# Kernel tuning notes

Measured on AMD Instinct MI355X. Metric: run time of the kernel, lower is better.

The kernel has to match this reference:

```python
import jax, jax.numpy as jnp
import numpy as np

N = 200000   # real nodes
P = 10       # num_parts (virtual nodes)
IN = 256     # in_channels
HID = 256    # hidden_channels
DCD = 256    # decode_channels (use_jk=False -> == hidden)
OUT = 64     # out_channels


def layer_norm(x, g, b, eps=1e-5):
    mu = jnp.mean(x, axis=-1, keepdims=True)
    var = jnp.var(x, axis=-1, keepdims=True)
    return (x - mu) * jax.lax.rsqrt(var + eps) * g + b


def setup_inputs() -> dict:
    key = jax.random.key(0)
    ks = jax.random.split(key, 16)
    s = lambda d: 1.0 / np.sqrt(d)
    return {
        "x": jax.random.normal(ks[0], (N + P, IN), dtype=jnp.float32),
        "mapping": jax.random.randint(ks[1], (N,), 0, P, dtype=jnp.int32),
        "vnode_embed": jax.random.normal(ks[2], (P, IN), dtype=jnp.float32),
        "vnode_bias_hid": 0.1 * jax.random.normal(ks[3], (P, HID), dtype=jnp.float32),
        "vnode_bias_dcd": 0.1 * jax.random.normal(ks[4], (P, DCD), dtype=jnp.float32),
        "W_in2hid": s(IN) * jax.random.normal(ks[5], (IN, HID), dtype=jnp.float32),
        "b_in2hid": jnp.zeros((HID,), dtype=jnp.float32),
        "g_ln_hid": jnp.ones((HID,), dtype=jnp.float32),
        "b_ln_hid": jnp.zeros((HID,), dtype=jnp.float32),
        "W_enc": s(HID) * jax.random.normal(ks[6], (HID, DCD), dtype=jnp.float32),
        "b_enc": jnp.zeros((DCD,), dtype=jnp.float32),
        "g_ln_enc": jnp.ones((DCD,), dtype=jnp.float32),
        "b_ln_enc": jnp.zeros((DCD,), dtype=jnp.float32),
        "W_aggr": s(2 * DCD) * jax.random.normal(ks[7], (2 * DCD, DCD), dtype=jnp.float32),
        "b_aggr": jnp.zeros((DCD,), dtype=jnp.float32),
        "W_out": s(DCD) * jax.random.normal(ks[8], (DCD, OUT), dtype=jnp.float32),
        "b_out": jnp.zeros((OUT,), dtype=jnp.float32),
    }


def reference(x, mapping, vnode_embed, vnode_bias_hid, vnode_bias_dcd,
              W_in2hid, b_in2hid, g_ln_hid, b_ln_hid,
              W_enc, b_enc, g_ln_enc, b_ln_enc,
              W_aggr, b_aggr, W_out, b_out):
    p = vnode_embed.shape[0]
    n = x.shape[0] - p
    # overwrite virtual-node rows with learned embeddings
    x = x.at[-p:].set(vnode_embed)
    # in2hid -> LayerNorm -> ELU
    x = jax.nn.elu(layer_norm(x @ W_in2hid + b_in2hid, g_ln_hid, b_ln_hid))
    x = x.at[-p:].add(vnode_bias_hid)
    # encoder stub: single linear hidden->decode with ELU (loss := 0)
    x = jax.nn.elu(x @ W_enc + b_enc)
    # decode-stage virtual-node bias
    x = x.at[-p:].add(vnode_bias_dcd)
    v_x = x[-p:]                      # [P, DCD]
    gathered = v_x[mapping]           # irregular gather of virtual rows, [N, DCD]
    n_x = jnp.concatenate([x[:n], gathered], axis=1)   # [N, 2*DCD]
    n_x = jax.nn.elu(layer_norm(n_x @ W_aggr + b_aggr, g_ln_enc, b_ln_enc))
    # dropout: eval mode -> identity
    full = jnp.concatenate([n_x, v_x], axis=0)
    y = full @ W_out + b_out
    out = y[:n]                       # [N, OUT]
    return out
```

## Files before the change

### kernel.cpp

```cpp
#include <hip/hip_runtime.h>
#include <hip/hip_bf16.h>
#include <math.h>

typedef unsigned short u16;
typedef unsigned int u32;
typedef __attribute__((ext_vector_type(8))) short bf16x8;
typedef __attribute__((ext_vector_type(4))) float f32x4;
typedef __attribute__((ext_vector_type(4))) int i32x4;

#define PV 10

__device__ __forceinline__ float bf2f(u16 u){
  union{unsigned int i; float f;} v; v.i = ((unsigned int)u)<<16; return v.f;
}
__device__ __forceinline__ u16 f2bf(float f){
  union{float f; unsigned int i;} v; v.f = f;
  unsigned int r = (v.i + 0x7FFFu + ((v.i>>16)&1u))>>16;
  return (u16)r;
}
__device__ __forceinline__ u32 cvtpk(float lo, float hi){
  u32 r; asm("v_cvt_pk_bf16_f32 %0, %1, %2" : "=v"(r) : "v"(lo), "v"(hi)); return r;
}
__device__ __forceinline__ float eluf(float z){
  return z > 0.f ? z : (__expf(z) - 1.f);
}
__device__ __forceinline__ float ldp(const void* p, int i, int f32f){
  return f32f ? ((const float*)p)[i] : bf2f(((const u16*)p)[i]);
}
__device__ __forceinline__ int swz(int row, int cb){
  int m = ((row & 7) << 4) ^ ((row & 8) << 2);
  return (row << 9) + (cb ^ m);
}

__global__ void k_sniff(const u16* __restrict__ x, int* __restrict__ flag){
  int t = threadIdx.x;
  u16 u = x[2*t];
  int e = (u >> 7) & 0xFF;
  int sane = (e >= 113 && e <= 134) ? 1 : 0;
  unsigned long long b = __ballot(sane);
  if (t == 0) *flag = (__popcll(b) < 32) ? 1 : 0;
}

__global__ void k_fragpack(const int* __restrict__ flagp,
                           const void* __restrict__ W1, const void* __restrict__ W2,
                           const void* __restrict__ Wa, const void* __restrict__ Wo,
                           u16* __restrict__ W1F, u16* __restrict__ W2F,
                           u16* __restrict__ WaF, u16* __restrict__ WoF)
{
  const int f = *flagp;
  int idx = blockIdx.x * 256 + threadIdx.x;
  if (idx < 196608) {
    int local = idx & 65535;
    int which = idx >> 16;
    int j = local & 7;
    int fid = local >> 3;
    int lane = fid & 63, q = lane & 15, g = lane >> 4;
    int n = (fid >> 6) & 3;
    int s = (fid >> 8) & 7;
    int w = (fid >> 11) & 3;
    int col = 64*w + 16*n + q;
    int k = 32*s + 8*g + j;
    const void* src = which == 0 ? W1 : (which == 1 ? W2 : Wa);
    u16* dst = which == 0 ? W1F : (which == 1 ? W2F : WaF);
    dst[local] = f2bf(ldp(src, k*256 + col, f));
  } else if (idx < 212992) {
    int local = idx - 196608;
    int j = local & 7;
    int fid = local >> 3;
    int lane = fid & 63, q = lane & 15, g = lane >> 4;
    int n = (fid >> 6) & 3;
    int s = (fid >> 8) & 7;
    int col = 16*n + q;
    int k = 32*s + 8*g + j;
    WoF[local] = f2bf(ldp(Wo, k*64 + col, f));
  }
}

__global__ void k_vnode(const int* __restrict__ flagp,
                        const void* __restrict__ embed, const void* __restrict__ W1,
                        const void* __restrict__ b1, const void* __restrict__ g1, const void* __restrict__ bb1,
                        const void* __restrict__ vbh,
                        const void* __restrict__ W2, const void* __restrict__ b2,
                        const void* __restrict__ vbd,
                        const void* __restrict__ Wa, const void* __restrict__ ba,
                        float* __restrict__ vg)
{
  __shared__ float buf[PV][256];
  __shared__ float st[PV][2];
  const int f = *flagp;
  const int t = threadIdx.x;
  const int lane = t & 63;
  const int w = t >> 6;

  for (int r=0;r<PV;r++) buf[r][t] = ldp(embed, r*256 + t, f);
  __syncthreads();

  float acc[PV];

  #pragma unroll
  for (int r=0;r<PV;r++) acc[r] = 0.f;
  for (int k8=0;k8<32;k8++){
    float wf[8];
    #pragma unroll
    for (int j=0;j<8;j++) wf[j] = ldp(W1, (k8*8+j)*256 + t, f);
    #pragma unroll
    for (int r=0;r<PV;r++){
      f32x4 a0 = *(const f32x4*)(&buf[r][k8*8]);
      f32x4 a1 = *(const f32x4*)(&buf[r][k8*8+4]);
      acc[r] = fmaf(a0[0],wf[0],acc[r]); acc[r] = fmaf(a0[1],wf[1],acc[r]);
      acc[r] = fmaf(a0[2],wf[2],acc[r]); acc[r] = fmaf(a0[3],wf[3],acc[r]);
      acc[r] = fmaf(a1[0],wf[4],acc[r]); acc[r] = fmaf(a1[1],wf[5],acc[r]);
      acc[r] = fmaf(a1[2],wf[6],acc[r]); acc[r] = fmaf(a1[3],wf[7],acc[r]);
    }
  }
  {
    float bv = ldp(b1, t, f);
    #pragma unroll
    for (int r=0;r<PV;r++) acc[r] += bv;
  }
  __syncthreads();
  #pragma unroll
  for (int r=0;r<PV;r++) buf[r][t] = acc[r];
  __syncthreads();
  for (int r = w; r < PV; r += 4){
    float v0=buf[r][lane], v1=buf[r][lane+64], v2=buf[r][lane+128], v3=buf[r][lane+192];
    float s = v0+v1+v2+v3;
    float ss = v0*v0+v1*v1+v2*v2+v3*v3;
    #pragma unroll
    for (int off=1; off<64; off<<=1){ s += __shfl_xor(s,off,64); ss += __shfl_xor(ss,off,64); }
    if (lane==0){
      float mu = s*(1.f/256.f);
      float var = ss*(1.f/256.f) - mu*mu;
      st[r][0]=mu; st[r][1]=rsqrtf(var+1e-5f);
    }
  }
  __syncthreads();
  {
    float gv = ldp(g1,t,f), bbv = ldp(bb1,t,f);
    #pragma unroll
    for (int r=0;r<PV;r++){
      float v = (acc[r]-st[r][0])*st[r][1]*gv + bbv;
      buf[r][t] = eluf(v) + ldp(vbh, r*256+t, f);
    }
  }
  __syncthreads();

  #pragma unroll
  for (int r=0;r<PV;r++) acc[r] = 0.f;
  for (int k8=0;k8<32;k8++){
    float wf[8];
    #pragma unroll
    for (int j=0;j<8;j++) wf[j] = ldp(W2, (k8*8+j)*256 + t, f);
    #pragma unroll
    for (int r=0;r<PV;r++){
      f32x4 a0 = *(const f32x4*)(&buf[r][k8*8]);
      f32x4 a1 = *(const f32x4*)(&buf[r][k8*8+4]);
      acc[r] = fmaf(a0[0],wf[0],acc[r]); acc[r] = fmaf(a0[1],wf[1],acc[r]);
      acc[r] = fmaf(a0[2],wf[2],acc[r]); acc[r] = fmaf(a0[3],wf[3],acc[r]);
      acc[r] = fmaf(a1[0],wf[4],acc[r]); acc[r] = fmaf(a1[1],wf[5],acc[r]);
      acc[r] = fmaf(a1[2],wf[6],acc[r]); acc[r] = fmaf(a1[3],wf[7],acc[r]);
    }
  }
  __syncthreads();
  {
    float bv = ldp(b2,t,f);
    #pragma unroll
    for (int r=0;r<PV;r++) buf[r][t] = eluf(acc[r]+bv) + ldp(vbd, r*256+t, f);
  }
  __syncthreads();

  #pragma unroll
  for (int r=0;r<PV;r++) acc[r] = 0.f;
  for (int k8=0;k8<32;k8++){
    float wf[8];
    #pragma unroll
    for (int j=0;j<8;j++) wf[j] = ldp(Wa, (256 + k8*8+j)*256 + t, f);
    #pragma unroll
    for (int r=0;r<PV;r++){
      f32x4 a0 = *(const f32x4*)(&buf[r][k8*8]);
      f32x4 a1 = *(const f32x4*)(&buf[r][k8*8+4]);
      acc[r] = fmaf(a0[0],wf[0],acc[r]); acc[r] = fmaf(a0[1],wf[1],acc[r]);
      acc[r] = fmaf(a0[2],wf[2],acc[r]); acc[r] = fmaf(a0[3],wf[3],acc[r]);
      acc[r] = fmaf(a1[0],wf[4],acc[r]); acc[r] = fmaf(a1[1],wf[5],acc[r]);
      acc[r] = fmaf(a1[2],wf[6],acc[r]); acc[r] = fmaf(a1[3],wf[7],acc[r]);
    }
  }
  {
    float bv = ldp(ba,t,f);
    #pragma unroll
    for (int r=0;r<PV;r++) vg[r*256+t] = acc[r] + bv;
  }
}

__device__ __forceinline__ void ln_rows(f32x4 (&acc)[4][4], float2 (*part)[4], float2* stats,
                                        int tid, int wid, int q, int g)
{
  #pragma unroll
  for (int m=0;m<4;m++){
    #pragma unroll
    for (int j=0;j<4;j++){
      float s1=0.f, s2=0.f;
      #pragma unroll
      for (int n=0;n<4;n++){ float v = acc[m][n][j]; s1+=v; s2+=v*v; }
      s1 += __shfl_xor(s1,1,64); s2 += __shfl_xor(s2,1,64);
      s1 += __shfl_xor(s1,2,64); s2 += __shfl_xor(s2,2,64);
      s1 += __shfl_xor(s1,4,64); s2 += __shfl_xor(s2,4,64);
      s1 += __shfl_xor(s1,8,64); s2 += __shfl_xor(s2,8,64);
      if (q == 0) part[16*m + 4*g + j][wid] = make_float2(s1, s2);
    }
  }
  __syncthreads();
  if (tid < 64){
    float s=0.f, ss=0.f;
    #pragma unroll
    for (int w=0;w<4;w++){ float2 p = part[tid][w]; s+=p.x; ss+=p.y; }
    float mu = s*(1.f/256.f);
    float var = ss*(1.f/256.f) - mu*mu;
    stats[tid] = make_float2(mu, rsqrtf(var + 1e-5f));
  }
  __syncthreads();
}

__global__ __launch_bounds__(256, 3) void k_main(
    const int* __restrict__ flagp,
    const void* __restrict__ x, const int* __restrict__ mapping,
    const void* __restrict__ b1, const void* __restrict__ g1, const void* __restrict__ bb1,
    const void* __restrict__ b2,
    const void* __restrict__ g3, const void* __restrict__ bb3,
    const void* __restrict__ bo,
    const u16* __restrict__ W1F, const u16* __restrict__ W2F,
    const u16* __restrict__ WaF, const u16* __restrict__ WoF,
    const float* __restrict__ vg, void* __restrict__ out)
{
  __shared__ __align__(16) u16 Abuf[64*256];
  __shared__ float2 part[64][4];
  __shared__ float2 stats[64];
  __shared__ int maplds[64];

  const int f = *flagp;
  const int tid = threadIdx.x;
  const int wid = tid >> 6;
  const int lane = tid & 63;
  const int q = lane & 15;
  const int g = lane >> 4;
  const int R0 = blockIdx.x * 64;

  if (f) {
    const float* xr = (const float*)x + (size_t)R0 * 256;
    #pragma unroll
    for (int i=0;i<8;i++){
      int c = tid + 256*i;
      int row = c >> 5;
      int cb  = (c & 31) << 4;
      int e0  = (c & 31) << 3;
      float4 a = *(const float4*)(xr + row*256 + e0);
      float4 b = *(const float4*)(xr + row*256 + e0 + 4);
      union { u32 u[4]; i32x4 v; } pk;
      pk.u[0]=cvtpk(a.x,a.y); pk.u[1]=cvtpk(a.z,a.w);
      pk.u[2]=cvtpk(b.x,b.y); pk.u[3]=cvtpk(b.z,b.w);
      *(i32x4*)((char*)Abuf + swz(row, cb)) = pk.v;
    }
  } else {
    const u16* xr = (const u16*)x + (size_t)R0 * 256;
    #pragma unroll
    for (int i=0;i<8;i++){
      int c = tid + 256*i;
      int row = c >> 5;
      int cb  = (c & 31) << 4;
      i32x4 v = *(const i32x4*)(xr + row*256 + ((c&31)<<3));
      *(i32x4*)((char*)Abuf + swz(row, cb)) = v;
    }
  }
  if (tid < 64){
    int mv = mapping[R0 + tid];
    maplds[tid] = mv < 0 ? 0 : (mv > PV-1 ? PV-1 : mv);
  }
  __syncthreads();

  f32x4 acc[4][4];
  const int fbase = wid*16384 + lane*8;

  {
    #pragma unroll
    for (int n=0;n<4;n++){
      float bv = ldp(b1, 64*wid + 16*n + q, f);
      #pragma unroll
      for (int m=0;m<4;m++) acc[m][n] = (f32x4){bv,bv,bv,bv};
    }
    #pragma unroll
    for (int s=0;s<8;s++){
      bf16x8 af[4], bw[4];
      #pragma unroll
      for (int m=0;m<4;m++) af[m] = *(const bf16x8*)((const char*)Abuf + swz(16*m+q, 64*s+16*g));
      #pragma unroll
      for (int n=0;n<4;n++) bw[n] = *(const bf16x8*)(W1F + fbase + (s*4+n)*512);
      #pragma unroll
      for (int m=0;m<4;m++){
        #pragma unroll
        for (int n=0;n<4;n++)
          acc[m][n] = __builtin_amdgcn_mfma_f32_16x16x32_bf16(af[m], bw[n], acc[m][n], 0,0,0);
      }
    }
  }
  ln_rows(acc, part, stats, tid, wid, q, g);
  {
    float gam[4], bet[4];
    #pragma unroll
    for (int n=0;n<4;n++){ int col = 64*wid+16*n+q; gam[n]=ldp(g1,col,f); bet[n]=ldp(bb1,col,f); }
    #pragma unroll
    for (int m=0;m<4;m++){
      #pragma unroll
      for (int n=0;n<4;n++){
        float v[4];
        #pragma unroll
        for (int j=0;j<4;j++){
          float2 st = stats[16*m + 4*g + j];
          v[j] = eluf((acc[m][n][j] - st.x) * st.y * gam[n] + bet[n]);
        }
        u32 u01 = cvtpk(v[0],v[1]), u23 = cvtpk(v[2],v[3]);
        int col2 = (64*wid+16*n+q)<<1;
        *(u16*)((char*)Abuf + swz(16*m+4*g+0, col2)) = (u16)u01;
        *(u16*)((char*)Abuf + swz(16*m+4*g+1, col2)) = (u16)(u01>>16);
        *(u16*)((char*)Abuf + swz(16*m+4*g+2, col2)) = (u16)u23;
        *(u16*)((char*)Abuf + swz(16*m+4*g+3, col2)) = (u16)(u23>>16);
      }
    }
  }
  __syncthreads();

  {
    #pragma unroll
    for (int n=0;n<4;n++){
      float bv = ldp(b2, 64*wid + 16*n + q, f);
      #pragma unroll
      for (int m=0;m<4;m++) acc[m][n] = (f32x4){bv,bv,bv,bv};
    }
    #pragma unroll
    for (int s=0;s<8;s++){
      bf16x8 af[4], bw[4];
      #pragma unroll
      for (int m=0;m<4;m++) af[m] = *(const bf16x8*)((const char*)Abuf + swz(16*m+q, 64*s+16*g));
      #pragma unroll
      for (int n=0;n<4;n++) bw[n] = *(const bf16x8*)(W2F + fbase + (s*4+n)*512);
      #pragma unroll
      for (int m=0;m<4;m++){
        #pragma unroll
        for (int n=0;n<4;n++)
          acc[m][n] = __builtin_amdgcn_mfma_f32_16x16x32_bf16(af[m], bw[n], acc[m][n], 0,0,0);
      }
    }
  }
  __syncthreads();
  {
    #pragma unroll
    for (int m=0;m<4;m++){
      #pragma unroll
      for (int n=0;n<4;n++){
        float v[4];
        #pragma unroll
        for (int j=0;j<4;j++) v[j] = eluf(acc[m][n][j]);
        u32 u01 = cvtpk(v[0],v[1]), u23 = cvtpk(v[2],v[3]);
        int col2 = (64*wid+16*n+q)<<1;
        *(u16*)((char*)Abuf + swz(16*m+4*g+0, col2)) = (u16)u01;
        *(u16*)((char*)Abuf + swz(16*m+4*g+1, col2)) = (u16)(u01>>16);
        *(u16*)((char*)Abuf + swz(16*m+4*g+2, col2)) = (u16)u23;
        *(u16*)((char*)Abuf + swz(16*m+4*g+3, col2)) = (u16)(u23>>16);
      }
    }
  }
  __syncthreads();

  {
    #pragma unroll
    for (int m=0;m<4;m++){
      int mp[4];
      #pragma unroll
      for (int j=0;j<4;j++) mp[j] = maplds[16*m + 4*g + j];
      #pragma unroll
      for (int n=0;n<4;n++){
        int col = 64*wid + 16*n + q;
        #pragma unroll
        for (int j=0;j<4;j++) acc[m][n][j] = vg[mp[j]*256 + col];
      }
    }
    #pragma unroll
    for (int s=0;s<8;s++){
      bf16x8 af[4], bw[4];
      #pragma unroll
      for (int m=0;m<4;m++) af[m] = *(const bf16x8*)((const char*)Abuf + swz(16*m+q, 64*s+16*g));
      #pragma unroll
      for (int n=0;n<4;n++) bw[n] = *(const bf16x8*)(WaF + fbase + (s*4+n)*512);
      #pragma unroll
      for (int m=0;m<4;m++){
        #pragma unroll
        for (int n=0;n<4;n++)
          acc[m][n] = __builtin_amdgcn_mfma_f32_16x16x32_bf16(af[m], bw[n], acc[m][n], 0,0,0);
      }
    }
  }
  ln_rows(acc, part, stats, tid, wid, q, g);
  {
    float gam[4], bet[4];
    #pragma unroll
    for (int n=0;n<4;n++){ int col = 64*wid+16*n+q; gam[n]=ldp(g3,col,f); bet[n]=ldp(bb3,col,f); }
    #pragma unroll
    for (int m=0;m<4;m++){
      #pragma unroll
      for (int n=0;n<4;n++){
        float v[4];
        #pragma unroll
        for (int j=0;j<4;j++){
          float2 st = stats[16*m + 4*g + j];
          v[j] = eluf((acc[m][n][j] - st.x) * st.y * gam[n] + bet[n]);
        }
        u32 u01 = cvtpk(v[0],v[1]), u23 = cvtpk(v[2],v[3]);
        int col2 = (64*wid+16*n+q)<<1;
        *(u16*)((char*)Abuf + swz(16*m+4*g+0, col2)) = (u16)u01;
        *(u16*)((char*)Abuf + swz(16*m+4*g+1, col2)) = (u16)(u01>>16);
        *(u16*)((char*)Abuf + swz(16*m+4*g+2, col2)) = (u16)u23;
        *(u16*)((char*)Abuf + swz(16*m+4*g+3, col2)) = (u16)(u23>>16);
      }
    }
  }
  __syncthreads();

  {
    f32x4 a4[4];
    #pragma unroll
    for (int n=0;n<4;n++){ float bv = ldp(bo, 16*n+q, f); a4[n] = (f32x4){bv,bv,bv,bv}; }
    #pragma unroll
    for (int s=0;s<8;s++){
      bf16x8 af = *(const bf16x8*)((const char*)Abuf + swz(16*wid+q, 64*s+16*g));
      #pragma unroll
      for (int n=0;n<4;n++){
        bf16x8 bw = *(const bf16x8*)(WoF + (s*4+n)*512 + lane*8);
        a4[n] = __builtin_amdgcn_mfma_f32_16x16x32_bf16(af, bw, a4[n], 0,0,0);
      }
    }
    if (f){
      __syncthreads();
      float* obuf = (float*)Abuf;
      #pragma unroll
      for (int n=0;n<4;n++){
        #pragma unroll
        for (int j=0;j<4;j++)
          obuf[(16*wid + 4*g + j)*68 + 16*n + q] = a4[n][j];
      }
      __syncthreads();
      int row = tid >> 2, c0 = (tid & 3) * 16;
      const float* src = obuf + row*68 + c0;
      float* dst = (float*)out + (size_t)(R0 + row)*64 + c0;
      f32x4 v0 = *(const f32x4*)(src);
      f32x4 v1 = *(const f32x4*)(src + 4);
      f32x4 v2 = *(const f32x4*)(src + 8);
      f32x4 v3 = *(const f32x4*)(src + 12);
      __builtin_nontemporal_store(v0, (f32x4*)(dst));
      __builtin_nontemporal_store(v1, (f32x4*)(dst + 4));
      __builtin_nontemporal_store(v2, (f32x4*)(dst + 8));
      __builtin_nontemporal_store(v3, (f32x4*)(dst + 12));
    } else {
      u16* outh = (u16*)out;
      #pragma unroll
      for (int n=0;n<4;n++){
        #pragma unroll
        for (int j=0;j<4;j++){
          int grow = R0 + 16*wid + 4*g + j;
          outh[(size_t)grow*64 + 16*n + q] = f2bf(a4[n][j]);
        }
      }
    }
  }
}

extern "C" void kernel_launch(void* const* d_in, const int* in_sizes, int n_in,
                              void* d_out, int out_size, void* d_ws, size_t ws_size,
                              hipStream_t stream)
{
  const void* x    = d_in[0];
  const int* mapping = (const int*)d_in[1];
  const void* embed= d_in[2];
  const void* vbh  = d_in[3];
  const void* vbd  = d_in[4];
  const void* W1   = d_in[5];
  const void* b1   = d_in[6];
  const void* g1   = d_in[7];
  const void* bb1  = d_in[8];
  const void* W2   = d_in[9];
  const void* b2   = d_in[10];
  const void* g3   = d_in[11];
  const void* bb3  = d_in[12];
  const void* Wa   = d_in[13];
  const void* ba   = d_in[14];
  const void* Wo   = d_in[15];
  const void* bo   = d_in[16];

  char* ws = (char*)d_ws;
  int* flagp = (int*)ws;
  u16* W1F = (u16*)(ws + 4096);
  u16* W2F = (u16*)(ws + 4096 + 131072);
  u16* WaF = (u16*)(ws + 4096 + 262144);
  u16* WoF = (u16*)(ws + 4096 + 393216);
  float* vg = (float*)(ws + 4096 + 425984);

  const int N = in_sizes[1];

  k_sniff<<<1, 64, 0, stream>>>((const u16*)x, flagp);
  k_fragpack<<<832, 256, 0, stream>>>(flagp, W1, W2, Wa, Wo, W1F, W2F, WaF, WoF);
  k_vnode<<<1, 256, 0, stream>>>(flagp, embed, W1, b1, g1, bb1, vbh, W2, b2, vbd, Wa, ba, vg);
  k_main<<<N/64, 256, 0, stream>>>(flagp, x, mapping, b1, g1, bb1, b2, g3, bb3, bo,
                                   W1F, W2F, WaF, WoF, vg, (void*)d_out);
}
```

Measured before the change: 352.5 us.

## Give each wave its own 16 rows and all 256 columns to drop block barriers

The main kernel is restructured so that each wave owns 16 rows and computes all 256 output columns itself, with a private 8KB LDS slice. Previously four waves split the columns of a 64-row tile. LayerNorm statistics are now reduced entirely with in-wave shuffles, which removes the cross-wave partial-sum buffer and every __syncthreads. The weight fragment packing is relaid out to match the new full-width per-wave access. In exchange, every wave must stream the full weight matrices from global/L2 instead of a quarter of them, and each A fragment is reused over 16 column tiles instead of 4.

New measurement: 413.2 us. 1.17x slower.

```diff
diff --git a/kernel.cpp b/kernel.cpp
--- a/kernel.cpp
+++ b/kernel.cpp
@@ -55,10 +55,9 @@
     int j = local & 7;
     int fid = local >> 3;
     int lane = fid & 63, q = lane & 15, g = lane >> 4;
-    int n = (fid >> 6) & 3;
-    int s = (fid >> 8) & 7;
-    int w = (fid >> 11) & 3;
-    int col = 64*w + 16*n + q;
+    int n = (fid >> 6) & 15;
+    int s = (fid >> 10) & 7;
+    int col = 16*n + q;
     int k = 32*s + 8*g + j;
     const void* src = which == 0 ? W1 : (which == 1 ? W2 : Wa);
     u16* dst = which == 0 ? W1F : (which == 1 ? W2F : WaF);
@@ -192,35 +191,6 @@
   }
 }
 
-__device__ __forceinline__ void ln_rows(f32x4 (&acc)[4][4], float2 (*part)[4], float2* stats,
-                                        int tid, int wid, int q, int g)
-{
-  #pragma unroll
-  for (int m=0;m<4;m++){
-    #pragma unroll
-    for (int j=0;j<4;j++){
-      float s1=0.f, s2=0.f;
-      #pragma unroll
-      for (int n=0;n<4;n++){ float v = acc[m][n][j]; s1+=v; s2+=v*v; }
-      s1 += __shfl_xor(s1,1,64); s2 += __shfl_xor(s2,1,64);
-      s1 += __shfl_xor(s1,2,64); s2 += __shfl_xor(s2,2,64);
-      s1 += __shfl_xor(s1,4,64); s2 += __shfl_xor(s2,4,64);
-      s1 += __shfl_xor(s1,8,64); s2 += __shfl_xor(s2,8,64);
-      if (q == 0) part[16*m + 4*g + j][wid] = make_float2(s1, s2);
-    }
-  }
-  __syncthreads();
-  if (tid < 64){
-    float s=0.f, ss=0.f;
-    #pragma unroll
-    for (int w=0;w<4;w++){ float2 p = part[tid][w]; s+=p.x; ss+=p.y; }
-    float mu = s*(1.f/256.f);
-    float var = ss*(1.f/256.f) - mu*mu;
-    stats[tid] = make_float2(mu, rsqrtf(var + 1e-5f));
-  }
-  __syncthreads();
-}
-
 __global__ __launch_bounds__(256, 3) void k_main(
     const int* __restrict__ flagp,
     const void* __restrict__ x, const int* __restrict__ mapping,
@@ -232,10 +202,7 @@
     const u16* __restrict__ WaF, const u16* __restrict__ WoF,
     const float* __restrict__ vg, void* __restrict__ out)
 {
-  __shared__ __align__(16) u16 Abuf[64*256];
-  __shared__ float2 part[64][4];
-  __shared__ float2 stats[64];
-  __shared__ int maplds[64];
+  __shared__ __align__(16) u16 Sall[4*4096];
 
   const int f = *flagp;
   const int tid = threadIdx.x;
@@ -243,186 +210,168 @@
   const int lane = tid & 63;
   const int q = lane & 15;
   const int g = lane >> 4;
-  const int R0 = blockIdx.x * 64;
-
-  if (f) {
-    const float* xr = (const float*)x + (size_t)R0 * 256;
-    #pragma unroll
-    for (int i=0;i<8;i++){
-      int c = tid + 256*i;
-      int row = c >> 5;
-      int cb  = (c & 31) << 4;
-      int e0  = (c & 31) << 3;
-      float4 a = *(const float4*)(xr + row*256 + e0);
-      float4 b = *(const float4*)(xr + row*256 + e0 + 4);
-      union { u32 u[4]; i32x4 v; } pk;
-      pk.u[0]=cvtpk(a.x,a.y); pk.u[1]=cvtpk(a.z,a.w);
-      pk.u[2]=cvtpk(b.x,b.y); pk.u[3]=cvtpk(b.z,b.w);
-      *(i32x4*)((char*)Abuf + swz(row, cb)) = pk.v;
-    }
-  } else {
-    const u16* xr = (const u16*)x + (size_t)R0 * 256;
-    #pragma unroll
-    for (int i=0;i<8;i++){
-      int c = tid + 256*i;
-      int row = c >> 5;
-      int cb  = (c & 31) << 4;
-      i32x4 v = *(const i32x4*)(xr + row*256 + ((c&31)<<3));
-      *(i32x4*)((char*)Abuf + swz(row, cb)) = v;
-    }
-  }
-  if (tid < 64){
-    int mv = mapping[R0 + tid];
-    maplds[tid] = mv < 0 ? 0 : (mv > PV-1 ? PV-1 : mv);
-  }
-  __syncthreads();
-
-  f32x4 acc[4][4];
-  const int fbase = wid*16384 + lane*8;
-
-  {
-    #pragma unroll
-    for (int n=0;n<4;n++){
-      float bv = ldp(b1, 64*wid + 16*n + q, f);
-      #pragma unroll
-      for (int m=0;m<4;m++) acc[m][n] = (f32x4){bv,bv,bv,bv};
-    }
+  const int R0 = blockIdx.x * 64 + wid * 16;
+  u16* S = Sall + wid * 4096;
+
+  {
+    int sr = lane >> 2;
+    int sc = (lane & 3) * 64;
+    if (f){
+      const float* xr = (const float*)x + (size_t)(R0 + sr)*256 + sc;
+      #pragma unroll
+      for (int i=0;i<8;i++){
+        float4 a = *(const float4*)(xr + i*8);
+        float4 b = *(const float4*)(xr + i*8 + 4);
+        union{ u32 u[4]; i32x4 v; } pk;
+        pk.u[0]=cvtpk(a.x,a.y); pk.u[1]=cvtpk(a.z,a.w);
+        pk.u[2]=cvtpk(b.x,b.y); pk.u[3]=cvtpk(b.z,b.w);
+        *(i32x4*)((char*)S + swz(sr, (sc + i*8)*2)) = pk.v;
+      }
+    } else {
+      const u16* xr = (const u16*)x + (size_t)(R0 + sr)*256 + sc;
+      #pragma unroll
+      for (int i=0;i<8;i++){
+        i32x4 v = *(const i32x4*)(xr + i*8);
+        *(i32x4*)((char*)S + swz(sr, (sc + i*8)*2)) = v;
+      }
+    }
+  }
+
+  f32x4 acc[16];
+
+  {
+    #pragma unroll
+    for (int n=0;n<16;n++){ float bv = ldp(b1, 16*n+q, f); acc[n] = (f32x4){bv,bv,bv,bv}; }
     #pragma unroll
     for (int s=0;s<8;s++){
-      bf16x8 af[4], bw[4];
-      #pragma unroll
-      for (int m=0;m<4;m++) af[m] = *(const bf16x8*)((const char*)Abuf + swz(16*m+q, 64*s+16*g));
-      #pragma unroll
-      for (int n=0;n<4;n++) bw[n] = *(const bf16x8*)(W1F + fbase + (s*4+n)*512);
-      #pragma unroll
-      for (int m=0;m<4;m++){
-        #pragma unroll
-        for (int n=0;n<4;n++)
-          acc[m][n] = __builtin_amdgcn_mfma_f32_16x16x32_bf16(af[m], bw[n], acc[m][n], 0,0,0);
-      }
-    }
-  }
-  ln_rows(acc, part, stats, tid, wid, q, g);
-  {
-    float gam[4], bet[4];
-    #pragma unroll
-    for (int n=0;n<4;n++){ int col = 64*wid+16*n+q; gam[n]=ldp(g1,col,f); bet[n]=ldp(bb1,col,f); }
-    #pragma unroll
-    for (int m=0;m<4;m++){
-      #pragma unroll
-      for (int n=0;n<4;n++){
-        float v[4];
-        #pragma unroll
-        for (int j=0;j<4;j++){
-          float2 st = stats[16*m + 4*g + j];
-          v[j] = eluf((acc[m][n][j] - st.x) * st.y * gam[n] + bet[n]);
-        }
-        u32 u01 = cvtpk(v[0],v[1]), u23 = cvtpk(v[2],v[3]);
-        int col2 = (64*wid+16*n+q)<<1;
-        *(u16*)((char*)Abuf + swz(16*m+4*g+0, col2)) = (u16)u01;
-        *(u16*)((char*)Abuf + swz(16*m+4*g+1, col2)) = (u16)(u01>>16);
-        *(u16*)((char*)Abuf + swz(16*m+4*g+2, col2)) = (u16)u23;
-        *(u16*)((char*)Abuf + swz(16*m+4*g+3, col2)) = (u16)(u23>>16);
-      }
-    }
-  }
-  __syncthreads();
-
-  {
-    #pragma unroll
-    for (int n=0;n<4;n++){
-      float bv = ldp(b2, 64*wid + 16*n + q, f);
-      #pragma unroll
-      for (int m=0;m<4;m++) acc[m][n] = (f32x4){bv,bv,bv,bv};
-    }
+      bf16x8 af = *(const bf16x8*)((const char*)S + swz(q, 64*s+16*g));
+      #pragma unroll
+      for (int nc=0;nc<4;nc++){
+        bf16x8 bw[4];
+        #pragma unroll
+        for (int u=0;u<4;u++) bw[u] = *(const bf16x8*)(W1F + (s*16+nc*4+u)*512 + lane*8);
+        #pragma unroll
+        for (int u=0;u<4;u++)
+          acc[nc*4+u] = __builtin_amdgcn_mfma_f32_16x16x32_bf16(af, bw[u], acc[nc*4+u], 0,0,0);
+      }
+    }
+  }
+  {
+    float mu_[4], rs_[4];
+    #pragma unroll
+    for (int j=0;j<4;j++){
+      float s1=0.f, s2=0.f;
+      #pragma unroll
+      for (int n=0;n<16;n++){ float v = acc[n][j]; s1+=v; s2+=v*v; }
+      s1 += __shfl_xor(s1,1,64); s2 += __shfl_xor(s2,1,64);
+      s1 += __shfl_xor(s1,2,64); s2 += __shfl_xor(s2,2,64);
+      s1 += __shfl_xor(s1,4,64); s2 += __shfl_xor(s2,4,64);
+      s1 += __shfl_xor(s1,8,64); s2 += __shfl_xor(s2,8,64);
+      float mu = s1*(1.f/256.f);
+      float var = s2*(1.f/256.f) - mu*mu;
+      mu_[j]=mu; rs_[j]=rsqrtf(var + 1e-5f);
+    }
+    #pragma unroll
+    for (int n=0;n<16;n++){
+      int col = 16*n+q;
+      float gam = ldp(g1,col,f), bet = ldp(bb1,col,f);
+      float v[4];
+      #pragma unroll
+      for (int j=0;j<4;j++) v[j] = eluf((acc[n][j]-mu_[j])*rs_[j]*gam + bet);
+      u32 u01 = cvtpk(v[0],v[1]), u23 = cvtpk(v[2],v[3]);
+      int c2 = col<<1;
+      *(u16*)((char*)S + swz(4*g+0, c2)) = (u16)u01;
+      *(u16*)((char*)S + swz(4*g+1, c2)) = (u16)(u01>>16);
+      *(u16*)((char*)S + swz(4*g+2, c2)) = (u16)u23;
+      *(u16*)((char*)S + swz(4*g+3, c2)) = (u16)(u23>>16);
+    }
+  }
+
+  {
+    #pragma unroll
+    for (int n=0;n<16;n++){ float bv = ldp(b2, 16*n+q, f); acc[n] = (f32x4){bv,bv,bv,bv}; }
     #pragma unroll
     for (int s=0;s<8;s++){
-      bf16x8 af[4], bw[4];
-      #pragma unroll
-      for (int m=0;m<4;m++) af[m] = *(const bf16x8*)((const char*)Abuf + swz(16*m+q, 64*s+16*g));
-      #pragma unroll
-      for (int n=0;n<4;n++) bw[n] = *(const bf16x8*)(W2F + fbase + (s*4+n)*512);
-      #pragma unroll
-      for (int m=0;m<4;m++){
-        #pragma unroll
-        for (int n=0;n<4;n++)
-          acc[m][n] = __builtin_amdgcn_mfma_f32_16x16x32_bf16(af[m], bw[n], acc[m][n], 0,0,0);
-      }
-    }
-  }
-  __syncthreads();
-  {
-    #pragma unroll
-    for (int m=0;m<4;m++){
-      #pragma unroll
-      for (int n=0;n<4;n++){
-        float v[4];
-        #pragma unroll
-        for (int j=0;j<4;j++) v[j] = eluf(acc[m][n][j]);
-        u32 u01 = cvtpk(v[0],v[1]), u23 = cvtpk(v[2],v[3]);
-        int col2 = (64*wid+16*n+q)<<1;
-        *(u16*)((char*)Abuf + swz(16*m+4*g+0, col2)) = (u16)u01;
-        *(u16*)((char*)Abuf + swz(16*m+4*g+1, col2)) = (u16)(u01>>16);
-        *(u16*)((char*)Abuf + swz(16*m+4*g+2, col2)) = (u16)u23;
-        *(u16*)((char*)Abuf + swz(16*m+4*g+3, col2)) = (u16)(u23>>16);
-      }
-    }
-  }
-  __syncthreads();
-
-  {
-    #pragma unroll
-    for (int m=0;m<4;m++){
-      int mp[4];
-      #pragma unroll
-      for (int j=0;j<4;j++) mp[j] = maplds[16*m + 4*g + j];
-      #pragma unroll
-      for (int n=0;n<4;n++){
-        int col = 64*wid + 16*n + q;
-        #pragma unroll
-        for (int j=0;j<4;j++) acc[m][n][j] = vg[mp[j]*256 + col];
-      }
+      bf16x8 af = *(const bf16x8*)((const char*)S + swz(q, 64*s+16*g));
+      #pragma unroll
+      for (int nc=0;nc<4;nc++){
+        bf16x8 bw[4];
+        #pragma unroll
+        for (int u=0;u<4;u++) bw[u] = *(const bf16x8*)(W2F + (s*16+nc*4+u)*512 + lane*8);
+        #pragma unroll
+        for (int u=0;u<4;u++)
+          acc[nc*4+u] = __builtin_amdgcn_mfma_f32_16x16x32_bf16(af, bw[u], acc[nc*4+u], 0,0,0);
+      }
+    }
+    #pragma unroll
+    for (int n=0;n<16;n++){
+      float v[4];
+      #pragma unroll
+      for (int j=0;j<4;j++) v[j] = eluf(acc[n][j]);
+      u32 u01 = cvtpk(v[0],v[1]), u23 = cvtpk(v[2],v[3]);
+      int c2 = (16*n+q)<<1;
+      *(u16*)((char*)S + swz(4*g+0, c2)) = (u16)u01;
+      *(u16*)((char*)S + swz(4*g+1, c2)) = (u16)(u01>>16);
+      *(u16*)((char*)S + swz(4*g+2, c2)) = (u16)u23;
+      *(u16*)((char*)S + swz(4*g+3, c2)) = (u16)(u23>>16);
+    }
+  }
+
+  {
+    int mp[4];
+    #pragma unroll
+    for (int j=0;j<4;j++){
+      int mv = mapping[R0 + 4*g + j];
+      mp[j] = mv < 0 ? 0 : (mv > PV-1 ? PV-1 : mv);
+    }
+    #pragma unroll
+    for (int n=0;n<16;n++){
+      int col = 16*n+q;
+      #pragma unroll
+      for (int j=0;j<4;j++) acc[n][j] = vg[mp[j]*256 + col];
     }
     #pragma unroll
     for (int s=0;s<8;s++){
-      bf16x8 af[4], bw[4];
-      #pragma unroll
-      for (int m=0;m<4;m++) af[m] = *(const bf16x8*)((const char*)Abuf + swz(16*m+q, 64*s+16*g));
-      #pragma unroll
-      for (int n=0;n<4;n++) bw[n] = *(const bf16x8*)(WaF + fbase + (s*4+n)*512);
-      #pragma unroll
-      for (int m=0;m<4;m++){
-        #pragma unroll
-        for (int n=0;n<4;n++)
-          acc[m][n] = __builtin_amdgcn_mfma_f32_16x16x32_bf16(af[m], bw[n], acc[m][n], 0,0,0);
-      }
-    }
-  }
-  ln_rows(acc, part, stats, tid, wid, q, g);
-  {
-    float gam[4], bet[4];
-    #pragma unroll
-    for (int n=0;n<4;n++){ int col = 64*wid+16*n+q; gam[n]=ldp(g3,col,f); bet[n]=ldp(bb3,col,f); }
-    #pragma unroll
-    for (int m=0;m<4;m++){
-      #pragma unroll
-      for (int n=0;n<4;n++){
-        float v[4];
-        #pragma unroll
-        for (int j=0;j<4;j++){
-          float2 st = stats[16*m + 4*g + j];
-          v[j] = eluf((acc[m][n][j] - st.x) * st.y * gam[n] + bet[n]);
-        }
-        u32 u01 = cvtpk(v[0],v[1]), u23 = cvtpk(v[2],v[3]);
-        int col2 = (64*wid+16*n+q)<<1;
-        *(u16*)((char*)Abuf + swz(16*m+4*g+0, col2)) = (u16)u01;
-        *(u16*)((char*)Abuf + swz(16*m+4*g+1, col2)) = (u16)(u01>>16);
-        *(u16*)((char*)Abuf + swz(16*m+4*g+2, col2)) = (u16)u23;
-        *(u16*)((char*)Abuf + swz(16*m+4*g+3, col2)) = (u16)(u23>>16);
-      }
-    }
-  }
-  __syncthreads();
+      bf16x8 af = *(const bf16x8*)((const char*)S + swz(q, 64*s+16*g));
+      #pragma unroll
+      for (int nc=0;nc<4;nc++){
+        bf16x8 bw[4];
+        #pragma unroll
+        for (int u=0;u<4;u++) bw[u] = *(const bf16x8*)(WaF + (s*16+nc*4+u)*512 + lane*8);
+        #pragma unroll
+        for (int u=0;u<4;u++)
+          acc[nc*4+u] = __builtin_amdgcn_mfma_f32_16x16x32_bf16(af, bw[u], acc[nc*4+u], 0,0,0);
+      }
+    }
+    float mu_[4], rs_[4];
+    #pragma unroll
+    for (int j=0;j<4;j++){
+      float s1=0.f, s2=0.f;
+      #pragma unroll
+      for (int n=0;n<16;n++){ float v = acc[n][j]; s1+=v; s2+=v*v; }
+      s1 += __shfl_xor(s1,1,64); s2 += __shfl_xor(s2,1,64);
+      s1 += __shfl_xor(s1,2,64); s2 += __shfl_xor(s2,2,64);
+      s1 += __shfl_xor(s1,4,64); s2 += __shfl_xor(s2,4,64);
+      s1 += __shfl_xor(s1,8,64); s2 += __shfl_xor(s2,8,64);
+      float mu = s1*(1.f/256.f);
+      float var = s2*(1.f/256.f) - mu*mu;
+      mu_[j]=mu; rs_[j]=rsqrtf(var + 1e-5f);
+    }
+    #pragma unroll
+    for (int n=0;n<16;n++){
+      int col = 16*n+q;
+      float gam = ldp(g3,col,f), bet = ldp(bb3,col,f);
+      float v[4];
+      #pragma unroll
+      for (int j=0;j<4;j++) v[j] = eluf((acc[n][j]-mu_[j])*rs_[j]*gam + bet);
+      u32 u01 = cvtpk(v[0],v[1]), u23 = cvtpk(v[2],v[3]);
+      int c2 = col<<1;
+      *(u16*)((char*)S + swz(4*g+0, c2)) = (u16)u01;
+      *(u16*)((char*)S + swz(4*g+1, c2)) = (u16)(u01>>16);
+      *(u16*)((char*)S + swz(4*g+2, c2)) = (u16)u23;
+      *(u16*)((char*)S + swz(4*g+3, c2)) = (u16)(u23>>16);
+    }
+  }
 
   {
     f32x4 a4[4];
@@ -430,7 +379,7 @@
     for (int n=0;n<4;n++){ float bv = ldp(bo, 16*n+q, f); a4[n] = (f32x4){bv,bv,bv,bv}; }
     #pragma unroll
     for (int s=0;s<8;s++){
-      bf16x8 af = *(const bf16x8*)((const char*)Abuf + swz(16*wid+q, 64*s+16*g));
+      bf16x8 af = *(const bf16x8*)((const char*)S + swz(q, 64*s+16*g));
       #pragma unroll
       for (int n=0;n<4;n++){
         bf16x8 bw = *(const bf16x8*)(WoF + (s*4+n)*512 + lane*8);
@@ -438,22 +387,20 @@
       }
     }
     if (f){
-      __syncthreads();
-      float* obuf = (float*)Abuf;
+      float* fb = (float*)S;
       #pragma unroll
       for (int n=0;n<4;n++){
         #pragma unroll
         for (int j=0;j<4;j++)
-          obuf[(16*wid + 4*g + j)*68 + 16*n + q] = a4[n][j];
-      }
-      __syncthreads();
-      int row = tid >> 2, c0 = (tid & 3) * 16;
-      const float* src = obuf + row*68 + c0;
-      float* dst = (float*)out + (size_t)(R0 + row)*64 + c0;
-      f32x4 v0 = *(const f32x4*)(src);
-      f32x4 v1 = *(const f32x4*)(src + 4);
-      f32x4 v2 = *(const f32x4*)(src + 8);
-      f32x4 v3 = *(const f32x4*)(src + 12);
+          fb[(4*g+j)*76 + 16*n + q] = a4[n][j];
+      }
+      int r = lane >> 2, c0 = (lane & 3) * 16;
+      const float* sp = fb + r*76 + c0;
+      f32x4 v0 = *(const f32x4*)(sp);
+      f32x4 v1 = *(const f32x4*)(sp + 4);
+      f32x4 v2 = *(const f32x4*)(sp + 8);
+      f32x4 v3 = *(const f32x4*)(sp + 12);
+      float* dst = (float*)out + (size_t)(R0 + r)*64 + c0;
       __builtin_nontemporal_store(v0, (f32x4*)(dst));
       __builtin_nontemporal_store(v1, (f32x4*)(dst + 4));
       __builtin_nontemporal_store(v2, (f32x4*)(dst + 8));
@@ -464,7 +411,7 @@
       for (int n=0;n<4;n++){
         #pragma unroll
         for (int j=0;j<4;j++){
-          int grow = R0 + 16*wid + 4*g + j;
+          int grow = R0 + 4*g + j;
           outh[(size_t)grow*64 + 16*n + q] = f2bf(a4[n][j]);
         }
       }
```
